# Performance work log

Measured on AMD Instinct MI355X. Metric: run time of the kernel, lower is better.

Reference implementation:

```python
import jax, jax.numpy as jnp
import numpy as np

EPS_COS = 1e-8   # torch cosine_similarity eps
EPS_DEN = 1e-6   # denominator eps in original loss
TEMP = 0.1


def setup_inputs() -> dict:
    key = jax.random.key(0)
    k1, _ = jax.random.split(key)
    N, D = 16384, 2048
    x = jax.random.normal(k1, (N, D), dtype=jnp.float32)
    pos_pair = jnp.arange(2, dtype=jnp.int64)  # (i, j) = (0, 1), i != j
    return {"x": x, "pos_pair": pos_pair}


def reference(x, pos_pair):
    # x: [N, D]; pos_pair: [2] int indices (i, j)
    i = pos_pair[0]
    j = pos_pair[1]
    xi = x[i]                                        # [D] anchor
    # cosine similarity of anchor against every row (single fused matvec)
    dots = x @ xi                                    # [N]
    norms = jnp.maximum(jnp.linalg.norm(x, axis=1), EPS_COS)   # [N]
    ni = jnp.maximum(jnp.linalg.norm(xi), EPS_COS)
    cos = dots / (norms * ni)                        # [N]
    e = jnp.exp(cos / TEMP)                          # [N]
    # denominator sums over all k != i (k == j included, as in original)
    mask = jnp.arange(x.shape[0]) != i
    denominator = jnp.sum(jnp.where(mask, e, 0.0))
    nominator = e[j]
    loss = -jnp.log(nominator / (denominator + EPS_DEN))
    return loss.reshape(1)  # original returns shape [1]
```

## Files before the change

### kernel.cpp

```cpp
#include <hip/hip_runtime.h>
#include <math.h>

#define D 2048
#define EPS_COS 1e-8f
#define EPS_DEN 1e-6f
#define INV_TEMP 10.0f

__device__ __forceinline__ void get_ij(const int* __restrict__ p, int n,
                                       int& i, int& j) {
    int i32 = p[0], j32 = p[1];
    if (i32 >= 0 && i32 < n && j32 >= 0 && j32 < n && i32 != j32) {
        i = i32; j = j32; return;
    }
    const long long* p64 = (const long long*)p;
    i = (int)p64[0]; j = (int)p64[1];
}

__global__ __launch_bounds__(256)
void row_kernel(const float* __restrict__ x, const int* __restrict__ pos,
                float* __restrict__ e_out, int n) {
    const int row = blockIdx.x;
    int i, j;
    get_ij(pos, n, i, j);

    const float4* __restrict__ xk = (const float4*)(x + (size_t)row * D);
    const float4* __restrict__ xi = (const float4*)(x + (size_t)i * D);

    float dot = 0.f, sqk = 0.f, sqi = 0.f;
    const int t = threadIdx.x;
#pragma unroll
    for (int it = 0; it < 2; ++it) {
        const int idx = t + it * 256;
        float4 a = xk[idx];
        float4 b = xi[idx];
        dot = fmaf(a.x, b.x, fmaf(a.y, b.y, fmaf(a.z, b.z, fmaf(a.w, b.w, dot))));
        sqk = fmaf(a.x, a.x, fmaf(a.y, a.y, fmaf(a.z, a.z, fmaf(a.w, a.w, sqk))));
        sqi = fmaf(b.x, b.x, fmaf(b.y, b.y, fmaf(b.z, b.z, fmaf(b.w, b.w, sqi))));
    }

#pragma unroll
    for (int off = 32; off > 0; off >>= 1) {
        dot += __shfl_down(dot, off);
        sqk += __shfl_down(sqk, off);
        sqi += __shfl_down(sqi, off);
    }

    __shared__ float s_dot[4], s_sqk[4], s_sqi[4];
    const int wave = t >> 6, lane = t & 63;
    if (lane == 0) { s_dot[wave] = dot; s_sqk[wave] = sqk; s_sqi[wave] = sqi; }
    __syncthreads();

    if (t == 0) {
        float dsum = s_dot[0] + s_dot[1] + s_dot[2] + s_dot[3];
        float ksum = s_sqk[0] + s_sqk[1] + s_sqk[2] + s_sqk[3];
        float isum = s_sqi[0] + s_sqi[1] + s_sqi[2] + s_sqi[3];
        float nk = fmaxf(sqrtf(ksum), EPS_COS);
        float ni = fmaxf(sqrtf(isum), EPS_COS);
        float cosv = dsum / (nk * ni);
        e_out[row] = expf(cosv * INV_TEMP);
    }
}

__global__ __launch_bounds__(1024)
void loss_kernel(const float* __restrict__ e, const int* __restrict__ pos,
                 float* __restrict__ out, int n) {
    int i, j;
    get_ij(pos, n, i, j);
    const int t = threadIdx.x;

    float s = 0.f;
    for (int k = t; k < n; k += 1024) s += e[k];

#pragma unroll
    for (int off = 32; off > 0; off >>= 1) s += __shfl_down(s, off);

    __shared__ float ls[16];
    if ((t & 63) == 0) ls[t >> 6] = s;
    __syncthreads();

    if (t == 0) {
        float tot = 0.f;
#pragma unroll
        for (int w = 0; w < 16; ++w) tot += ls[w];
        float den = tot - e[i];
        float nom = e[j];
        out[0] = -logf(nom / (den + EPS_DEN));
    }
}

extern "C" void kernel_launch(void* const* d_in, const int* in_sizes, int n_in,
                              void* d_out, int out_size, void* d_ws, size_t ws_size,
                              hipStream_t stream) {
    const float* x   = (const float*)d_in[0];
    const int*   pos = (const int*)d_in[1];
    float*       out = (float*)d_out;
    float*       e   = (float*)d_ws;

    const int n = in_sizes[0] / D;

    row_kernel<<<n, 256, 0, stream>>>(x, pos, e, n);
    loss_kernel<<<1, 1024, 0, stream>>>(e, pos, out, n);
}
```

Before: 190.8 us.

## Fuse row cosine and loss reduction into one persistent wave-per-row kernel

Replaces the per-row block kernel and the single-block loss kernel with one persistent grid kernel. Each wave handles whole rows in a grid-stride loop, keeps the anchor row in registers so it is loaded once per wave, and accumulates the denominator locally. A last-block-done atomic counter then computes the final loss. This removes the second launch, the intermediate e buffer and the repeated anchor reloads. In exchange it adds a memset launch, float atomics whose summation order is nondeterministic, and a 2048-block grid that may limit memory-level parallelism.

```diff
diff --git a/kernel.cpp b/kernel.cpp
--- a/kernel.cpp
+++ b/kernel.cpp
@@ -5,6 +5,10 @@
 #define EPS_COS 1e-8f
 #define EPS_DEN 1e-6f
 #define INV_TEMP 10.0f
+#define TPB 256
+#define NBLOCKS 2048
+#define WPB (TPB / 64)
+#define NWAVES (NBLOCKS * WPB)
 
 __device__ __forceinline__ void get_ij(const int* __restrict__ p, int n,
                                        int& i, int& j) {
@@ -16,75 +20,76 @@
     i = (int)p64[0]; j = (int)p64[1];
 }
 
-__global__ __launch_bounds__(256)
-void row_kernel(const float* __restrict__ x, const int* __restrict__ pos,
-                float* __restrict__ e_out, int n) {
-    const int row = blockIdx.x;
+__global__ __launch_bounds__(TPB)
+void fused_kernel(const float* __restrict__ x, const int* __restrict__ pos,
+                  float* __restrict__ out, float* __restrict__ acc, int n) {
     int i, j;
     get_ij(pos, n, i, j);
+    const int lane  = threadIdx.x & 63;
+    const int wave  = threadIdx.x >> 6;
+    const int gwave = blockIdx.x * WPB + wave;
 
-    const float4* __restrict__ xk = (const float4*)(x + (size_t)row * D);
     const float4* __restrict__ xi = (const float4*)(x + (size_t)i * D);
+    float4 b[8];
+#pragma unroll
+    for (int w = 0; w < 8; ++w) b[w] = xi[lane + w * 64];
 
-    float dot = 0.f, sqk = 0.f, sqi = 0.f;
-    const int t = threadIdx.x;
+    float sqi = 0.f;
 #pragma unroll
-    for (int it = 0; it < 2; ++it) {
-        const int idx = t + it * 256;
-        float4 a = xk[idx];
-        float4 b = xi[idx];
-        dot = fmaf(a.x, b.x, fmaf(a.y, b.y, fmaf(a.z, b.z, fmaf(a.w, b.w, dot))));
-        sqk = fmaf(a.x, a.x, fmaf(a.y, a.y, fmaf(a.z, a.z, fmaf(a.w, a.w, sqk))));
-        sqi = fmaf(b.x, b.x, fmaf(b.y, b.y, fmaf(b.z, b.z, fmaf(b.w, b.w, sqi))));
+    for (int w = 0; w < 8; ++w)
+        sqi = fmaf(b[w].x, b[w].x, fmaf(b[w].y, b[w].y,
+              fmaf(b[w].z, b[w].z, fmaf(b[w].w, b[w].w, sqi))));
+#pragma unroll
+    for (int off = 32; off; off >>= 1) sqi += __shfl_down(sqi, off);
+    const float ni = fmaxf(sqrtf(sqi), EPS_COS);
+
+    float local_den = 0.f;
+    float local_ej  = 0.f;
+
+    for (int row = gwave; row < n; row += NWAVES) {
+        const float4* __restrict__ xk = (const float4*)(x + (size_t)row * D);
+        float4 a[8];
+#pragma unroll
+        for (int w = 0; w < 8; ++w) a[w] = xk[lane + w * 64];
+        float dot = 0.f, sq = 0.f;
+#pragma unroll
+        for (int w = 0; w < 8; ++w) {
+            dot = fmaf(a[w].x, b[w].x, fmaf(a[w].y, b[w].y,
+                  fmaf(a[w].z, b[w].z, fmaf(a[w].w, b[w].w, dot))));
+            sq  = fmaf(a[w].x, a[w].x, fmaf(a[w].y, a[w].y,
+                  fmaf(a[w].z, a[w].z, fmaf(a[w].w, a[w].w, sq))));
+        }
+#pragma unroll
+        for (int off = 32; off; off >>= 1) {
+            dot += __shfl_down(dot, off);
+            sq  += __shfl_down(sq,  off);
+        }
+        if (lane == 0) {
+            float nk = fmaxf(sqrtf(sq), EPS_COS);
+            float e  = expf(INV_TEMP * dot / (nk * ni));
+            if (row != i) local_den += e;
+            if (row == j) local_ej = e;
+        }
     }
 
+    __shared__ float s_den[WPB];
+    if (lane == 0) {
+        s_den[wave] = local_den;
+        if (local_ej != 0.f) atomicAdd(&acc[1], local_ej);
+    }
+    __syncthreads();
+    if (threadIdx.x == 0) {
+        float bden = 0.f;
 #pragma unroll
-    for (int off = 32; off > 0; off >>= 1) {
-        dot += __shfl_down(dot, off);
-        sqk += __shfl_down(sqk, off);
-        sqi += __shfl_down(sqi, off);
-    }
-
-    __shared__ float s_dot[4], s_sqk[4], s_sqi[4];
-    const int wave = t >> 6, lane = t & 63;
-    if (lane == 0) { s_dot[wave] = dot; s_sqk[wave] = sqk; s_sqi[wave] = sqi; }
-    __syncthreads();
-
-    if (t == 0) {
-        float dsum = s_dot[0] + s_dot[1] + s_dot[2] + s_dot[3];
-        float ksum = s_sqk[0] + s_sqk[1] + s_sqk[2] + s_sqk[3];
-        float isum = s_sqi[0] + s_sqi[1] + s_sqi[2] + s_sqi[3];
-        float nk = fmaxf(sqrtf(ksum), EPS_COS);
-        float ni = fmaxf(sqrtf(isum), EPS_COS);
-        float cosv = dsum / (nk * ni);
-        e_out[row] = expf(cosv * INV_TEMP);
-    }
-}
-
-__global__ __launch_bounds__(1024)
-void loss_kernel(const float* __restrict__ e, const int* __restrict__ pos,
-                 float* __restrict__ out, int n) {
-    int i, j;
-    get_ij(pos, n, i, j);
-    const int t = threadIdx.x;
-
-    float s = 0.f;
-    for (int k = t; k < n; k += 1024) s += e[k];
-
-#pragma unroll
-    for (int off = 32; off > 0; off >>= 1) s += __shfl_down(s, off);
-
-    __shared__ float ls[16];
-    if ((t & 63) == 0) ls[t >> 6] = s;
-    __syncthreads();
-
-    if (t == 0) {
-        float tot = 0.f;
-#pragma unroll
-        for (int w = 0; w < 16; ++w) tot += ls[w];
-        float den = tot - e[i];
-        float nom = e[j];
-        out[0] = -logf(nom / (den + EPS_DEN));
+        for (int w = 0; w < WPB; ++w) bden += s_den[w];
+        atomicAdd(&acc[0], bden);
+        __threadfence();
+        unsigned old = atomicAdd((unsigned*)&acc[2], 1u);
+        if (old == gridDim.x - 1) {
+            float den = atomicAdd(&acc[0], 0.f);
+            float ej  = atomicAdd(&acc[1], 0.f);
+            out[0] = -logf(ej / (den + EPS_DEN));
+        }
     }
 }
 
@@ -94,10 +99,10 @@
     const float* x   = (const float*)d_in[0];
     const int*   pos = (const int*)d_in[1];
     float*       out = (float*)d_out;
-    float*       e   = (float*)d_ws;
+    float*       acc = (float*)d_ws;
 
     const int n = in_sizes[0] / D;
 
-    row_kernel<<<n, 256, 0, stream>>>(x, pos, e, n);
-    loss_kernel<<<1, 1024, 0, stream>>>(e, pos, out, n);
+    hipMemsetAsync(d_ws, 0, 16, stream);
+    fused_kernel<<<NBLOCKS, TPB, 0, stream>>>(x, pos, out, acc, n);
 }
```

Measured after the change: 284.6 us. +49.1%, slower.
